# Performance work log

Hardware: AMD Instinct MI355X
Metric: run time of the kernel (lower is better)

The kernel has to match this reference:

```python
import jax, jax.numpy as jnp
import numpy as np

TM, TK = 64, 64
M, K = 4096, 4096
N_BLOCKS = 1024
T_SHAPE = (1, 2048, K)


def _gelu_tanh(x):
    # Matches the Triton kernel's tanh-approx GELU:
    inner = 0.7978845608 * (x + 0.044715 * x * x * x)
    return x * 0.5 * (1.0 + jnp.tanh(inner))


def setup_inputs() -> dict:
    key = jax.random.key(0)
    k1, k2, k3, k4, k5 = jax.random.split(key, 5)
    x = jax.random.normal(k1, T_SHAPE, dtype=jnp.float32)
    values = jax.random.normal(k2, (N_BLOCKS, TM, TK), dtype=jnp.float32) * 0.02
    bias = jax.random.normal(k3, (M,), dtype=jnp.float32) * 0.02
    block_rows = jax.random.randint(k4, (N_BLOCKS,), 0, M // TM, dtype=jnp.int32)
    block_cols = jax.random.randint(k5, (N_BLOCKS,), 0, K // TK, dtype=jnp.int32)
    return {"x": x, "values": values, "bias": bias,
            "block_rows": block_rows, "block_cols": block_cols}


def reference(x, values, bias, block_rows, block_cols):
    # y = gelu(W_sparse @ x^T + bias[:, None])^T, W stored as 64x64 blocks.
    in_features = x.shape[-1]
    out_features = bias.shape[0]
    n_row_blocks = out_features // TM
    x_flat = x.reshape(-1, in_features)          # [T, K]
    T = x_flat.shape[0]
    xb = x_flat.reshape(T, in_features // TK, TK)  # [T, nKblk, TK]
    g = xb[:, block_cols, :]                     # [T, nb, TK] gather per block col
    # per-block small GEMM: values[n] @ g[t, n]^T -> [nb, T, TM]
    partial = jnp.einsum('nmk,tnk->ntm', values, g)
    # scatter-add block contributions into their output row blocks
    outb = jax.ops.segment_sum(partial, block_rows, num_segments=n_row_blocks)
    y = outb.transpose(1, 0, 2).reshape(T, out_features)  # [T, M]
    y = _gelu_tanh(y + bias[None, :])
    return y.reshape(x.shape[:-1] + (out_features,))
```

## Files before the change

### kernel.cpp

```cpp
#include <hip/hip_runtime.h>
#include <hip/hip_bf16.h>

#define K_DIM 4096
#define M_DIM 4096
#define T_DIM 2048
#define NB    1024
#define BT    64

typedef __attribute__((ext_vector_type(8))) short bf16x8;
typedef __attribute__((ext_vector_type(4))) float f32x4;

__device__ __forceinline__ unsigned short f2bf(float f) {
    unsigned int u = __builtin_bit_cast(unsigned int, f);
    unsigned int r = (u + 0x7FFFu + ((u >> 16) & 1u)) >> 16;
    return (unsigned short)r;
}

__global__ __launch_bounds__(256, 2) void fsl_mfma_kernel(
    const float* __restrict__ x, const float* __restrict__ values,
    const float* __restrict__ bias, const int* __restrict__ brows,
    const int* __restrict__ bcols, float* __restrict__ out)
{
    __shared__ __align__(16) unsigned char sA[2][64 * 128];
    __shared__ __align__(16) unsigned char sB[2][64 * 128];
    __shared__ int s_list[NB];
    __shared__ int s_cnt;

    const int tid = threadIdx.x;
    const int r   = blockIdx.x >> 5;
    const int t0  = (blockIdx.x & 31) * BT;

    if (tid == 0) s_cnt = 0;
    __syncthreads();
    for (int n = tid; n < NB; n += 256) {
        if (brows[n] == r) {
            int p = atomicAdd(&s_cnt, 1);
            s_list[p] = n;
        }
    }
    __syncthreads();
    const int cnt = s_cnt;

    const int wave = tid >> 6;
    const int lane = tid & 63;
    const int wt   = wave >> 1;
    const int wm   = wave & 1;
    const int lrow = lane & 15;
    const int lk8  = (lane >> 4) * 8;

    const int srow = tid >> 4;
    const int scol = tid & 15;

    f32x4 acc[2][2] = {};
    float4 ra[4], rb[4];

    auto stage_load = [&](int i) {
        const int n = s_list[i];
        const int c = bcols[n];
        const float* xp = x + (size_t)(t0 + srow) * K_DIM + c * 64 + scol * 4;
        const float* vp = values + (size_t)n * 4096 + srow * 64 + scol * 4;
#pragma unroll
        for (int j = 0; j < 4; ++j) {
            ra[j] = *(const float4*)(xp + (size_t)(j * 16) * K_DIM);
            rb[j] = *(const float4*)(vp + j * 16 * 64);
        }
    };

    auto stage_write = [&](int buf) {
#pragma unroll
        for (int j = 0; j < 4; ++j) {
            const int row = srow + j * 16;
            int byte = row * 128 + scol * 8;
            byte ^= (row & 7) << 4;
            uint2 pa, pb;
            pa.x = (unsigned int)f2bf(ra[j].x) | ((unsigned int)f2bf(ra[j].y) << 16);
            pa.y = (unsigned int)f2bf(ra[j].z) | ((unsigned int)f2bf(ra[j].w) << 16);
            pb.x = (unsigned int)f2bf(rb[j].x) | ((unsigned int)f2bf(rb[j].y) << 16);
            pb.y = (unsigned int)f2bf(rb[j].z) | ((unsigned int)f2bf(rb[j].w) << 16);
            *(uint2*)(&sA[buf][byte]) = pa;
            *(uint2*)(&sB[buf][byte]) = pb;
        }
    };

    auto compute = [&](int buf) {
#pragma unroll
        for (int ks = 0; ks < 2; ++ks) {
            bf16x8 a[2], b[2];
#pragma unroll
            for (int f = 0; f < 2; ++f) {
                const int trow = wt * 32 + f * 16 + lrow;
                int abyte = trow * 128 + (ks * 32 + lk8) * 2;
                abyte ^= (trow & 7) << 4;
                a[f] = *(const bf16x8*)(&sA[buf][abyte]);
                const int mrow = wm * 32 + f * 16 + lrow;
                int bbyte = mrow * 128 + (ks * 32 + lk8) * 2;
                bbyte ^= (mrow & 7) << 4;
                b[f] = *(const bf16x8*)(&sB[buf][bbyte]);
            }
#pragma unroll
            for (int ft = 0; ft < 2; ++ft)
#pragma unroll
                for (int fm = 0; fm < 2; ++fm)
                    acc[ft][fm] = __builtin_amdgcn_mfma_f32_16x16x32_bf16(
                        a[ft], b[fm], acc[ft][fm], 0, 0, 0);
        }
    };

    if (cnt > 0) { stage_load(0); stage_write(0); }
    for (int i = 0; i < cnt; ++i) {
        __syncthreads();
        const bool more = (i + 1 < cnt);
        if (more) stage_load(i + 1);
        compute(i & 1);
        if (more) stage_write((i + 1) & 1);
    }

    const int mcol  = lane & 15;
    const int trow4 = (lane >> 4) * 4;
#pragma unroll
    for (int ft = 0; ft < 2; ++ft) {
#pragma unroll
        for (int fm = 0; fm < 2; ++fm) {
            const int mg = r * 64 + wm * 32 + fm * 16 + mcol;
            const float bv = bias[mg];
#pragma unroll
            for (int reg = 0; reg < 4; ++reg) {
                const int t = t0 + wt * 32 + ft * 16 + trow4 + reg;
                float v = acc[ft][fm][reg] + bv;
                float inner = 0.7978845608f * (v + 0.044715f * v * v * v);
                inner = fminf(fmaxf(inner, -15.0f), 15.0f);
                const float e  = __expf(2.0f * inner);
                const float th = 1.0f - 2.0f / (e + 1.0f);
                out[(size_t)t * M_DIM + mg] = v * 0.5f * (1.0f + th);
            }
        }
    }
}

extern "C" void kernel_launch(void* const* d_in, const int* in_sizes, int n_in,
                              void* d_out, int out_size, void* d_ws, size_t ws_size,
                              hipStream_t stream) {
    const float* x      = (const float*)d_in[0];
    const float* values = (const float*)d_in[1];
    const float* bias   = (const float*)d_in[2];
    const int*   brows  = (const int*)d_in[3];
    const int*   bcols  = (const int*)d_in[4];
    float* out = (float*)d_out;

    dim3 grid(64 * 32);
    fsl_mfma_kernel<<<grid, 256, 0, stream>>>(x, values, bias, brows, bcols, out);
}
```

Before: 170.2 us.

## Pre-convert inputs to bf16 and stream tiles via global_load_lds with XCD-aware mapping

Adds two pre-pass kernels that convert x and values to bf16 in workspace once. The main kernel then loads bf16 tiles directly into LDS with global_load_lds, which removes the per-block fp32 loads and per-tile conversion. It also remaps blocks so that blocks sharing a row block land on the same XCD, for better L2 reuse. The cost is two extra launches and a full read and write pass over x and values, and the fp32 path is kept as a fallback when the workspace is too small.

```diff
diff --git a/kernel.cpp b/kernel.cpp
--- a/kernel.cpp
+++ b/kernel.cpp
@@ -5,7 +5,6 @@
 #define M_DIM 4096
 #define T_DIM 2048
 #define NB    1024
-#define BT    64
 
 typedef __attribute__((ext_vector_type(8))) short bf16x8;
 typedef __attribute__((ext_vector_type(4))) float f32x4;
@@ -16,7 +15,139 @@
     return (unsigned short)r;
 }
 
-__global__ __launch_bounds__(256, 2) void fsl_mfma_kernel(
+__device__ __forceinline__ void gld16(const void* g, void* l) {
+    __builtin_amdgcn_global_load_lds(
+        (const __attribute__((address_space(1))) unsigned int*)g,
+        (__attribute__((address_space(3))) unsigned int*)l, 16, 0, 0);
+}
+
+__global__ __launch_bounds__(256) void cvt_bf16_kernel(
+    const float* __restrict__ in, uint4* __restrict__ outp, int n8)
+{
+    int i = blockIdx.x * 256 + threadIdx.x;
+    if (i >= n8) return;
+    const float4* p = (const float4*)in + 2 * (size_t)i;
+    float4 a = p[0];
+    float4 b = p[1];
+    uint4 w;
+    w.x = (unsigned)f2bf(a.x) | ((unsigned)f2bf(a.y) << 16);
+    w.y = (unsigned)f2bf(a.z) | ((unsigned)f2bf(a.w) << 16);
+    w.z = (unsigned)f2bf(b.x) | ((unsigned)f2bf(b.y) << 16);
+    w.w = (unsigned)f2bf(b.z) | ((unsigned)f2bf(b.w) << 16);
+    outp[i] = w;
+}
+
+__global__ __launch_bounds__(256, 2) void fsl_mfma_bf16_kernel(
+    const unsigned short* __restrict__ xb, const unsigned short* __restrict__ vb,
+    const float* __restrict__ bias, const int* __restrict__ brows,
+    const int* __restrict__ bcols, float* __restrict__ out)
+{
+    __shared__ __align__(16) unsigned char sA[2][64 * 128];
+    __shared__ __align__(16) unsigned char sB[2][64 * 128];
+    __shared__ unsigned int s_list[NB];
+    __shared__ int s_cnt;
+
+    const int tid  = threadIdx.x;
+    const int b    = blockIdx.x;
+    const int xcd  = b & 7;
+    const int slot = b >> 3;
+    const int t0   = (xcd + 8 * (slot & 3)) * 64;
+    const int r    = slot >> 2;
+
+    if (tid == 0) s_cnt = 0;
+    __syncthreads();
+    for (int n = tid; n < NB; n += 256) {
+        if (brows[n] == r) {
+            int p = atomicAdd(&s_cnt, 1);
+            s_list[p] = (unsigned)n | ((unsigned)bcols[n] << 16);
+        }
+    }
+    __syncthreads();
+    const int cnt = s_cnt;
+
+    const int wave = tid >> 6;
+    const int lane = tid & 63;
+    const int wt   = wave >> 1;
+    const int wm   = wave & 1;
+    const int lrow = lane & 15;
+    const int lk8  = (lane >> 4) * 8;
+
+    f32x4 acc[2][2] = {};
+
+    const int srr    = lane >> 3;
+    const int scol16 = lane & 7;
+
+    auto stage = [&](int i, int buf) {
+        const unsigned int pc = s_list[i];
+        const int n = pc & 0xFFFF;
+        const int c = pc >> 16;
+#pragma unroll
+        for (int ch = 0; ch < 2; ++ch) {
+            const int rbase = wave * 16 + ch * 8;
+            const int row   = rbase + srr;
+            const int sc    = (scol16 ^ (row & 7)) * 8;
+            gld16(xb + (size_t)(t0 + row) * K_DIM + c * 64 + sc,
+                  &sA[buf][rbase * 128]);
+            gld16(vb + (size_t)n * 4096 + row * 64 + sc,
+                  &sB[buf][rbase * 128]);
+        }
+    };
+
+    auto compute = [&](int buf) {
+#pragma unroll
+        for (int ks = 0; ks < 2; ++ks) {
+            bf16x8 a[2], bfr[2];
+#pragma unroll
+            for (int f = 0; f < 2; ++f) {
+                const int trow = wt * 32 + f * 16 + lrow;
+                int abyte = trow * 128 + (ks * 32 + lk8) * 2;
+                abyte ^= (trow & 7) << 4;
+                a[f] = *(const bf16x8*)(&sA[buf][abyte]);
+                const int mrow = wm * 32 + f * 16 + lrow;
+                int bbyte = mrow * 128 + (ks * 32 + lk8) * 2;
+                bbyte ^= (mrow & 7) << 4;
+                bfr[f] = *(const bf16x8*)(&sB[buf][bbyte]);
+            }
+#pragma unroll
+            for (int ft = 0; ft < 2; ++ft)
+#pragma unroll
+                for (int fm = 0; fm < 2; ++fm)
+                    acc[ft][fm] = __builtin_amdgcn_mfma_f32_16x16x32_bf16(
+                        a[ft], bfr[fm], acc[ft][fm], 0, 0, 0);
+        }
+    };
+
+    if (cnt > 0) stage(0, 0);
+    __syncthreads();
+    for (int i = 0; i < cnt; ++i) {
+        if (i + 1 < cnt) stage(i + 1, (i + 1) & 1);
+        compute(i & 1);
+        __syncthreads();
+    }
+
+    const int mcol  = lane & 15;
+    const int trow4 = (lane >> 4) * 4;
+#pragma unroll
+    for (int ft = 0; ft < 2; ++ft) {
+#pragma unroll
+        for (int fm = 0; fm < 2; ++fm) {
+            const int mg = r * 64 + wm * 32 + fm * 16 + mcol;
+            const float bv = bias[mg];
+#pragma unroll
+            for (int reg = 0; reg < 4; ++reg) {
+                const int t = t0 + wt * 32 + ft * 16 + trow4 + reg;
+                float v = acc[ft][fm][reg] + bv;
+                float inner = 0.7978845608f * (v + 0.044715f * v * v * v);
+                inner = fminf(fmaxf(inner, -15.0f), 15.0f);
+                const float e  = __expf(2.0f * inner);
+                const float th = 1.0f - 2.0f / (e + 1.0f);
+                out[(size_t)t * M_DIM + mg] = v * 0.5f * (1.0f + th);
+            }
+        }
+    }
+}
+
+__global__ __launch_bounds__(256, 2) void fsl_mfma_fallback(
     const float* __restrict__ x, const float* __restrict__ values,
     const float* __restrict__ bias, const int* __restrict__ brows,
     const int* __restrict__ bcols, float* __restrict__ out)
@@ -28,7 +159,7 @@
 
     const int tid = threadIdx.x;
     const int r   = blockIdx.x >> 5;
-    const int t0  = (blockIdx.x & 31) * BT;
+    const int t0  = (blockIdx.x & 31) * 64;
 
     if (tid == 0) s_cnt = 0;
     __syncthreads();
@@ -47,7 +178,6 @@
     const int wm   = wave & 1;
     const int lrow = lane & 15;
     const int lk8  = (lane >> 4) * 8;
-
     const int srow = tid >> 4;
     const int scol = tid & 15;
 
@@ -65,7 +195,6 @@
             rb[j] = *(const float4*)(vp + j * 16 * 64);
         }
     };
-
     auto stage_write = [&](int buf) {
 #pragma unroll
         for (int j = 0; j < 4; ++j) {
@@ -73,19 +202,18 @@
             int byte = row * 128 + scol * 8;
             byte ^= (row & 7) << 4;
             uint2 pa, pb;
-            pa.x = (unsigned int)f2bf(ra[j].x) | ((unsigned int)f2bf(ra[j].y) << 16);
-            pa.y = (unsigned int)f2bf(ra[j].z) | ((unsigned int)f2bf(ra[j].w) << 16);
-            pb.x = (unsigned int)f2bf(rb[j].x) | ((unsigned int)f2bf(rb[j].y) << 16);
-            pb.y = (unsigned int)f2bf(rb[j].z) | ((unsigned int)f2bf(rb[j].w) << 16);
+            pa.x = (unsigned)f2bf(ra[j].x) | ((unsigned)f2bf(ra[j].y) << 16);
+            pa.y = (unsigned)f2bf(ra[j].z) | ((unsigned)f2bf(ra[j].w) << 16);
+            pb.x = (unsigned)f2bf(rb[j].x) | ((unsigned)f2bf(rb[j].y) << 16);
+            pb.y = (unsigned)f2bf(rb[j].z) | ((unsigned)f2bf(rb[j].w) << 16);
             *(uint2*)(&sA[buf][byte]) = pa;
             *(uint2*)(&sB[buf][byte]) = pb;
         }
     };
-
     auto compute = [&](int buf) {
 #pragma unroll
         for (int ks = 0; ks < 2; ++ks) {
-            bf16x8 a[2], b[2];
+            bf16x8 a[2], bb[2];
 #pragma unroll
             for (int f = 0; f < 2; ++f) {
                 const int trow = wt * 32 + f * 16 + lrow;
@@ -95,14 +223,14 @@
                 const int mrow = wm * 32 + f * 16 + lrow;
                 int bbyte = mrow * 128 + (ks * 32 + lk8) * 2;
                 bbyte ^= (mrow & 7) << 4;
-                b[f] = *(const bf16x8*)(&sB[buf][bbyte]);
+                bb[f] = *(const bf16x8*)(&sB[buf][bbyte]);
             }
 #pragma unroll
             for (int ft = 0; ft < 2; ++ft)
 #pragma unroll
                 for (int fm = 0; fm < 2; ++fm)
                     acc[ft][fm] = __builtin_amdgcn_mfma_f32_16x16x32_bf16(
-                        a[ft], b[fm], acc[ft][fm], 0, 0, 0);
+                        a[ft], bb[fm], acc[ft][fm], 0, 0, 0);
         }
     };
 
@@ -147,6 +275,21 @@
     const int*   bcols  = (const int*)d_in[4];
     float* out = (float*)d_out;
 
-    dim3 grid(64 * 32);
-    fsl_mfma_kernel<<<grid, 256, 0, stream>>>(x, values, bias, brows, bcols, out);
-}
+    const size_t x_elems = (size_t)T_DIM * K_DIM;
+    const size_t v_elems = (size_t)NB * 64 * 64;
+    const size_t ws_need = (x_elems + v_elems) * 2;
+
+    if (ws_size >= ws_need) {
+        unsigned short* xb = (unsigned short*)d_ws;
+        unsigned short* vb = xb + x_elems;
+        const int n8x = (int)(x_elems / 8);
+        const int n8v = (int)(v_elems / 8);
+        cvt_bf16_kernel<<<(n8x + 255) / 256, 256, 0, stream>>>(x, (uint4*)xb, n8x);
+        cvt_bf16_kernel<<<(n8v + 255) / 256, 256, 0, stream>>>(values, (uint4*)vb, n8v);
+        fsl_mfma_bf16_kernel<<<dim3(64 * 32), 256, 0, stream>>>(
+            xb, vb, bias, brows, bcols, out);
+    } else {
+        fsl_mfma_fallback<<<dim3(64 * 32), 256, 0, stream>>>(
+            x, values, bias, brows, bcols, out);
+    }
+}
```

After: 142.8 us. -16.1%, faster.
